# Optimization experiments

Hardware: AMD Instinct MI355X
Metric: run time of the kernel (lower is better)

The kernel has to match this reference:

```python
import jax, jax.numpy as jnp
import numpy as np

KERNEL_SIZE = 9
SIGMA_SPATIAL = 3.0
SIGMA_RANGE = 0.1
RADIUS = KERNEL_SIZE // 2


def setup_inputs() -> dict:
    key = jax.random.key(0)
    image = jax.random.uniform(key, (4096, 4096), dtype=jnp.float32)
    return {"image": image}


def reference(image):
    # Bilateral filter: out[i,j] = sum_w(spatial*range*window) / sum_w(spatial*range)
    H, W = image.shape
    r = RADIUS
    sigma_s_sq = 2.0 * SIGMA_SPATIAL ** 2
    sigma_r_sq = 2.0 * SIGMA_RANGE ** 2
    padded = jnp.pad(image, r, mode='reflect')  # (H+2r, W+2r)
    num = jnp.zeros_like(image)
    den = jnp.zeros_like(image)
    # Fixed 9x9 tap loop (81 iterations, unrolled by jit); fully vectorized over pixels.
    for dy in range(KERNEL_SIZE):
        for dx in range(KERNEL_SIZE):
            win = padded[dy:dy + H, dx:dx + W]  # (H, W) shifted window tap
            spatial_w = np.float32(np.exp(-((dx - r) ** 2 + (dy - r) ** 2) / sigma_s_sq))
            w = spatial_w * jnp.exp(-(win - image) ** 2 / sigma_r_sq)
            num = num + w * win
            den = den + w
    # Center tap weight is always 1, so den > 0 everywhere; plain divide matches torch branch.
    return num / den
```

## Files before the change

kernel.cpp:

```cpp
#include <hip/hip_runtime.h>

#define IMG_H 4096
#define IMG_W 4096
#define RAD 4
#define TSX 64
#define TSY 16
#define LROWS (TSY + 2*RAD)
#define LCOLS (TSX + 2*RAD)

__device__ __forceinline__ int reflect_idx(int i, int n) {
    i = (i < 0) ? -i : i;
    i = (i >= n) ? (2 * n - 2 - i) : i;
    return i;
}

__global__ __launch_bounds__(256, 8) void bilateral_kernel(const float* __restrict__ in,
                                                           float* __restrict__ out) {
    __shared__ float tile[LROWS * LCOLS];
    const int bx = blockIdx.x * TSX;
    const int by = blockIdx.y * TSY;
    const int tid = threadIdx.x;

    const bool interior = (blockIdx.x > 0) && (blockIdx.x < (int)gridDim.x - 1) &&
                          (blockIdx.y > 0) && (blockIdx.y < (int)gridDim.y - 1);
    if (interior) {
        const float* src = in + (size_t)(by - RAD) * IMG_W + (bx - RAD);
#pragma unroll
        for (int it = 0; it < 2; ++it) {
            int i = tid + it * 256;
            if (i < 432) {
                int row = i / 18;
                int col = i - row * 18;
                float4 q = *reinterpret_cast<const float4*>(src + row * IMG_W + col * 4);
                *reinterpret_cast<float4*>(&tile[row * 72 + col * 4]) = q;
            }
        }
    } else {
        for (int i = tid; i < LROWS * LCOLS; i += 256) {
            int ly = i / 72;
            int lx = i - ly * 72;
            int gy = reflect_idx(by + ly - RAD, IMG_H);
            int gx = reflect_idx(bx + lx - RAD, IMG_W);
            tile[ly * 72 + lx] = in[gy * IMG_W + gx];
        }
    }
    __syncthreads();

    const int tx = tid & 15;
    const int ty = tid >> 4;
    const int x0 = tx * 4;

    constexpr float LOG2E  = 1.4426950408889634f;
    constexpr float KR     = -50.0f * LOG2E;
    constexpr float S23    = 8388608.0f;
    constexpr float KRS    = KR * S23;
    constexpr float NEG2KRS = -2.0f * KRS;
    constexpr float SC_COEF = -LOG2E / 18.0f;
    constexpr float BIAS   = (127.0f - 0.04303f) * S23;

    float B[4];
    {
        float4 c4 = *reinterpret_cast<const float4*>(&tile[(ty + RAD) * 72 + x0 + RAD]);
        B[0] = NEG2KRS * c4.x;
        B[1] = NEG2KRS * c4.y;
        B[2] = NEG2KRS * c4.z;
        B[3] = NEG2KRS * c4.w;
    }

    float n[4] = {0.f, 0.f, 0.f, 0.f};
    float d[4] = {0.f, 0.f, 0.f, 0.f};
    const float* rowp = &tile[ty * 72 + x0];

#pragma unroll 1
    for (int dy = 0; dy < 9; ++dy) {
        float4 q0 = *reinterpret_cast<const float4*>(rowp);
        float4 q1 = *reinterpret_cast<const float4*>(rowp + 4);
        float4 q2 = *reinterpret_cast<const float4*>(rowp + 8);
        rowp += 72;
        float v[12] = {q0.x, q0.y, q0.z, q0.w,
                       q1.x, q1.y, q1.z, q1.w,
                       q2.x, q2.y, q2.z, q2.w};

        int e = dy - 4;
        float fy = __builtin_amdgcn_exp2f(SC_COEF * (float)(e * e));

        float rn[4], rd[4];
#pragma unroll
        for (int dx = 0; dx < 9; ++dx) {
            const int dd = (dx - 4) * (dx - 4);
            const float scb = (float)dd * (SC_COEF * S23) + BIAS;
#pragma unroll
            for (int p = 0; p < 4; ++p) {
                float vv = v[dx + p];
                float t  = fmaf(KRS, vv, B[p]);
                float aa = fmaf(vv, t, scb);
                float w  = __int_as_float((int)aa);
                if (dx == 0) { rn[p] = w * vv; rd[p] = w; }
                else         { rn[p] = fmaf(w, vv, rn[p]); rd[p] += w; }
            }
        }
#pragma unroll
        for (int p = 0; p < 4; ++p) {
            n[p] = fmaf(fy, rn[p], n[p]);
            d[p] = fmaf(fy, rd[p], d[p]);
        }
    }

    float4 o;
    o.x = n[0] * __builtin_amdgcn_rcpf(d[0]);
    o.y = n[1] * __builtin_amdgcn_rcpf(d[1]);
    o.z = n[2] * __builtin_amdgcn_rcpf(d[2]);
    o.w = n[3] * __builtin_amdgcn_rcpf(d[3]);
    *reinterpret_cast<float4*>(&out[(size_t)(by + ty) * IMG_W + bx + x0]) = o;
}

extern "C" void kernel_launch(void* const* d_in, const int* in_sizes, int n_in,
                              void* d_out, int out_size, void* d_ws, size_t ws_size,
                              hipStream_t stream) {
    const float* in = (const float*)d_in[0];
    float* out = (float*)d_out;
    dim3 grid(IMG_W / TSX, IMG_H / TSY);
    bilateral_kernel<<<grid, 256, 0, stream>>>(in, out);
}
```

Before: 257.2 us.

## Compute eight pixels per thread and fold row spatial weight into exp bias

Doubles the tile width to 128 so each thread computes 8 horizontally adjacent pixels. Each thread now loads 20 values per window row instead of 12, which cuts shared-memory loads per pixel. The per-row spatial factor is folded into the exponent bias, so the separate exp2 and the per-row rescale of partial sums go away and accumulation runs straight into n/d. The cost is more registers per thread, with launch bounds lowered to 6 waves, and fewer blocks overall.

```diff
diff --git a/kernel.cpp b/kernel.cpp
--- a/kernel.cpp
+++ b/kernel.cpp
@@ -3,8 +3,9 @@
 #define IMG_H 4096
 #define IMG_W 4096
 #define RAD 4
-#define TSX 64
+#define TSX 128
 #define TSY 16
+#define NPX 8
 #define LROWS (TSY + 2*RAD)
 #define LCOLS (TSX + 2*RAD)
 
@@ -14,7 +15,7 @@
     return i;
 }
 
-__global__ __launch_bounds__(256, 8) void bilateral_kernel(const float* __restrict__ in,
+__global__ __launch_bounds__(256, 6) void bilateral_kernel(const float* __restrict__ in,
                                                            float* __restrict__ out) {
     __shared__ float tile[LROWS * LCOLS];
     const int bx = blockIdx.x * TSX;
@@ -26,92 +27,100 @@
     if (interior) {
         const float* src = in + (size_t)(by - RAD) * IMG_W + (bx - RAD);
 #pragma unroll
-        for (int it = 0; it < 2; ++it) {
+        for (int it = 0; it < 4; ++it) {
             int i = tid + it * 256;
-            if (i < 432) {
-                int row = i / 18;
-                int col = i - row * 18;
+            if (i < 816) {
+                int row = i / 34;
+                int col = i - row * 34;
                 float4 q = *reinterpret_cast<const float4*>(src + row * IMG_W + col * 4);
-                *reinterpret_cast<float4*>(&tile[row * 72 + col * 4]) = q;
+                *reinterpret_cast<float4*>(&tile[row * 136 + col * 4]) = q;
             }
         }
     } else {
         for (int i = tid; i < LROWS * LCOLS; i += 256) {
-            int ly = i / 72;
-            int lx = i - ly * 72;
+            int ly = i / 136;
+            int lx = i - ly * 136;
             int gy = reflect_idx(by + ly - RAD, IMG_H);
             int gx = reflect_idx(bx + lx - RAD, IMG_W);
-            tile[ly * 72 + lx] = in[gy * IMG_W + gx];
+            tile[ly * 136 + lx] = in[gy * IMG_W + gx];
         }
     }
     __syncthreads();
 
     const int tx = tid & 15;
     const int ty = tid >> 4;
-    const int x0 = tx * 4;
+    const int x0 = tx * NPX;
 
-    constexpr float LOG2E  = 1.4426950408889634f;
-    constexpr float KR     = -50.0f * LOG2E;
-    constexpr float S23    = 8388608.0f;
-    constexpr float KRS    = KR * S23;
+    constexpr float LOG2E = 1.4426950408889634f;
+    constexpr float KR  = -50.0f * LOG2E;
+    constexpr float S23 = 8388608.0f;
+    constexpr float KRS = KR * S23;
     constexpr float NEG2KRS = -2.0f * KRS;
-    constexpr float SC_COEF = -LOG2E / 18.0f;
-    constexpr float BIAS   = (127.0f - 0.04303f) * S23;
+    constexpr float SCS = (-LOG2E / 18.0f) * S23;
+    constexpr float BIAS = (127.0f - 0.04303f) * S23;
 
-    float B[4];
+    float B[NPX], n[NPX], d[NPX];
     {
-        float4 c4 = *reinterpret_cast<const float4*>(&tile[(ty + RAD) * 72 + x0 + RAD]);
-        B[0] = NEG2KRS * c4.x;
-        B[1] = NEG2KRS * c4.y;
-        B[2] = NEG2KRS * c4.z;
-        B[3] = NEG2KRS * c4.w;
+        float4 c0 = *reinterpret_cast<const float4*>(&tile[(ty + RAD) * 136 + x0 + 4]);
+        float4 c1 = *reinterpret_cast<const float4*>(&tile[(ty + RAD) * 136 + x0 + 8]);
+        B[0] = NEG2KRS * c0.x; B[1] = NEG2KRS * c0.y;
+        B[2] = NEG2KRS * c0.z; B[3] = NEG2KRS * c0.w;
+        B[4] = NEG2KRS * c1.x; B[5] = NEG2KRS * c1.y;
+        B[6] = NEG2KRS * c1.z; B[7] = NEG2KRS * c1.w;
     }
+#pragma unroll
+    for (int p = 0; p < NPX; ++p) { n[p] = 0.f; d[p] = 0.f; }
 
-    float n[4] = {0.f, 0.f, 0.f, 0.f};
-    float d[4] = {0.f, 0.f, 0.f, 0.f};
-    const float* rowp = &tile[ty * 72 + x0];
+    const float* rowp = &tile[ty * 136 + x0];
 
 #pragma unroll 1
-    for (int dy = 0; dy < 9; ++dy) {
+    for (int r = 0; r < 9; ++r) {
         float4 q0 = *reinterpret_cast<const float4*>(rowp);
         float4 q1 = *reinterpret_cast<const float4*>(rowp + 4);
         float4 q2 = *reinterpret_cast<const float4*>(rowp + 8);
-        rowp += 72;
-        float v[12] = {q0.x, q0.y, q0.z, q0.w,
-                       q1.x, q1.y, q1.z, q1.w,
-                       q2.x, q2.y, q2.z, q2.w};
+        float4 q3 = *reinterpret_cast<const float4*>(rowp + 12);
+        float4 q4 = *reinterpret_cast<const float4*>(rowp + 16);
+        rowp += 136;
+        float v[20] = {q0.x, q0.y, q0.z, q0.w, q1.x, q1.y, q1.z, q1.w,
+                       q2.x, q2.y, q2.z, q2.w, q3.x, q3.y, q3.z, q3.w,
+                       q4.x, q4.y, q4.z, q4.w};
 
-        int e = dy - 4;
-        float fy = __builtin_amdgcn_exp2f(SC_COEF * (float)(e * e));
-
-        float rn[4], rd[4];
+        int e = r - 4;
+        float syf = (float)(e * e) * SCS;
+        float scb[9];
 #pragma unroll
         for (int dx = 0; dx < 9; ++dx) {
             const int dd = (dx - 4) * (dx - 4);
-            const float scb = (float)dd * (SC_COEF * S23) + BIAS;
+            scb[dx] = syf + ((float)dd * SCS + BIAS);
+        }
+
 #pragma unroll
-            for (int p = 0; p < 4; ++p) {
+        for (int dx = 0; dx < 9; ++dx) {
+#pragma unroll
+            for (int p = 0; p < NPX; ++p) {
                 float vv = v[dx + p];
                 float t  = fmaf(KRS, vv, B[p]);
-                float aa = fmaf(vv, t, scb);
+                float aa = fmaf(vv, t, scb[dx]);
                 float w  = __int_as_float((int)aa);
-                if (dx == 0) { rn[p] = w * vv; rd[p] = w; }
-                else         { rn[p] = fmaf(w, vv, rn[p]); rd[p] += w; }
+                n[p] = fmaf(w, vv, n[p]);
+                d[p] += w;
             }
-        }
-#pragma unroll
-        for (int p = 0; p < 4; ++p) {
-            n[p] = fmaf(fy, rn[p], n[p]);
-            d[p] = fmaf(fy, rd[p], d[p]);
         }
     }
 
-    float4 o;
-    o.x = n[0] * __builtin_amdgcn_rcpf(d[0]);
-    o.y = n[1] * __builtin_amdgcn_rcpf(d[1]);
-    o.z = n[2] * __builtin_amdgcn_rcpf(d[2]);
-    o.w = n[3] * __builtin_amdgcn_rcpf(d[3]);
-    *reinterpret_cast<float4*>(&out[(size_t)(by + ty) * IMG_W + bx + x0]) = o;
+    float4 o0, o1;
+    o0.x = n[0] * __builtin_amdgcn_rcpf(d[0]);
+    o0.y = n[1] * __builtin_amdgcn_rcpf(d[1]);
+    o0.z = n[2] * __builtin_amdgcn_rcpf(d[2]);
+    o0.w = n[3] * __builtin_amdgcn_rcpf(d[3]);
+    o1.x = n[4] * __builtin_amdgcn_rcpf(d[4]);
+    o1.y = n[5] * __builtin_amdgcn_rcpf(d[5]);
+    o1.z = n[6] * __builtin_amdgcn_rcpf(d[6]);
+    o1.w = n[7] * __builtin_amdgcn_rcpf(d[7]);
+
+    float* orow = &out[(size_t)(by + ty) * IMG_W + bx + x0];
+    *reinterpret_cast<float4*>(orow)     = o0;
+    *reinterpret_cast<float4*>(orow + 4) = o1;
 }
 
 extern "C" void kernel_launch(void* const* d_in, const int* in_sizes, int n_in,
```

Result: slower. 854.6 us (+232.3%).
